# Performance work log

Measured on AMD Instinct MI355X. Metric: run time of the kernel, lower is better.

Reference implementation:

```python
import jax, jax.numpy as jnp
import numpy as np

COMMITMENT_COST = 0.25


def setup_inputs() -> dict:
    key = jax.random.key(0)
    k1, k2 = jax.random.split(key)
    B, T, D = 32, 256, 512
    K = 8192
    x = jax.random.normal(k1, (B, T, D), dtype=jnp.float32)
    # nn.Embedding init: uniform(-1/K, 1/K)
    embeddings = jax.random.uniform(k2, (K, D), dtype=jnp.float32,
                                    minval=-1.0 / K, maxval=1.0 / K)
    return {"x": x, "embeddings": embeddings}


def reference(x, embeddings):
    orig_shape = x.shape
    D = orig_shape[-1]
    x_flat = x.reshape(-1, D)                      # [N, D]

    # squared Euclidean distances via expansion (argmin-equivalent to cdist)
    x_sq = jnp.sum(x_flat * x_flat, axis=1, keepdims=True)     # [N, 1]
    e_sq = jnp.sum(embeddings * embeddings, axis=1)            # [K]
    dots = jnp.einsum('nd,kd->nk', x_flat, embeddings)         # [N, K]
    distances = x_sq - 2.0 * dots + e_sq[None, :]              # [N, K]

    indices = jnp.argmin(distances, axis=1)                    # [N]
    quantized = embeddings[indices].reshape(orig_shape)        # [..., D]
    indices = indices.reshape(orig_shape[:-1])

    commitment_loss = jnp.mean((x - jax.lax.stop_gradient(quantized)) ** 2) * COMMITMENT_COST
    codebook_loss = jnp.mean((quantized - jax.lax.stop_gradient(x)) ** 2)
    total_loss = commitment_loss + codebook_loss

    # straight-through estimator
    quantized_st = x + jax.lax.stop_gradient(quantized - x)
    return quantized_st, indices, commitment_loss, codebook_loss, total_loss
```

## Files before the change

### kernel.cpp

```cpp
#include <hip/hip_runtime.h>

#define N_ROWS 8192
#define K_CODES 8192
#define D_DIM 512

typedef unsigned long long u64;

__global__ __launch_bounds__(256) void vq_sq(const float* __restrict__ x,
                                             const float* __restrict__ emb,
                                             float* __restrict__ x_sq,
                                             float* __restrict__ e_sq) {
  const int t = threadIdx.x;
  const int wave = t >> 6, l = t & 63;
  const int half = l >> 5, ll = l & 31;
  const int q = ll >> 3, j = ll & 7;
  const int row = blockIdx.x * 8 + wave * 2 + half;
  const float* p =
      (row < N_ROWS) ? (x + (size_t)row * D_DIM)
                     : (emb + (size_t)(row - N_ROWS) * D_DIM);
  const float v0 = p[128 * q + j];
  float r = __fmul_rn(v0, v0);
#pragma unroll
  for (int i = 1; i < 16; ++i) {
    const float v = p[128 * q + 8 * i + j];
    r = __fadd_rn(r, __fmul_rn(v, v));
  }
  r = __fadd_rn(r, __shfl_xor(r, 1, 64));
  r = __fadd_rn(r, __shfl_xor(r, 2, 64));
  r = __fadd_rn(r, __shfl_xor(r, 4, 64));
  r = __fadd_rn(r, __shfl_xor(r, 8, 64));
  r = __fadd_rn(r, __shfl_xor(r, 16, 64));
  if (ll == 0) {
    if (row < N_ROWS) x_sq[row] = r;
    else e_sq[row - N_ROWS] = r;
  }
}

__device__ __forceinline__ void compute_chunk16(const float* __restrict__ esb,
                                                const float* __restrict__ xw,
                                                int dd0, int lane,
                                                float (&acc)[8][4]) {
  const int lbase = lane * 16;
  const int lm = (lane >> 1) & 3;
#pragma unroll
  for (int g = 0; g < 4; ++g) {
    const float* p = esb + lbase + 4 * (g ^ lm);
    const float4 ev0 = *reinterpret_cast<const float4*>(p);
    const float4 ev1 = *reinterpret_cast<const float4*>(p + 1024);
    const float4 ev2 = *reinterpret_cast<const float4*>(p + 2048);
    const float4 ev3 = *reinterpret_cast<const float4*>(p + 3072);
#pragma unroll
    for (int r = 0; r < 8; ++r) {
      const float4 xv =
          *reinterpret_cast<const float4*>(xw + r * D_DIM + dd0 + 4 * g);
      float a0 = acc[r][0], a1 = acc[r][1], a2 = acc[r][2], a3 = acc[r][3];
      a0 = __fmaf_rn(xv.x, ev0.x, a0);
      a0 = __fmaf_rn(xv.y, ev0.y, a0);
      a0 = __fmaf_rn(xv.z, ev0.z, a0);
      a0 = __fmaf_rn(xv.w, ev0.w, a0);
      a1 = __fmaf_rn(xv.x, ev1.x, a1);
      a1 = __fmaf_rn(xv.y, ev1.y, a1);
      a1 = __fmaf_rn(xv.z, ev1.z, a1);
      a1 = __fmaf_rn(xv.w, ev1.w, a1);
      a2 = __fmaf_rn(xv.x, ev2.x, a2);
      a2 = __fmaf_rn(xv.y, ev2.y, a2);
      a2 = __fmaf_rn(xv.z, ev2.z, a2);
      a2 = __fmaf_rn(xv.w, ev2.w, a2);
      a3 = __fmaf_rn(xv.x, ev3.x, a3);
      a3 = __fmaf_rn(xv.y, ev3.y, a3);
      a3 = __fmaf_rn(xv.z, ev3.z, a3);
      a3 = __fmaf_rn(xv.w, ev3.w, a3);
      acc[r][0] = a0; acc[r][1] = a1; acc[r][2] = a2; acc[r][3] = a3;
    }
  }
}

#define STAGE(BUF, ESRC)                                                       \
  do {                                                                         \
    __builtin_amdgcn_global_load_lds(                                          \
        (const __attribute__((address_space(1))) void*)(ESRC),                 \
        (__attribute__((address_space(3))) void*)(&es[BUF][4 * t]), 16, 0, 0); \
    __builtin_amdgcn_global_load_lds(                                          \
        (const __attribute__((address_space(1))) void*)((ESRC) + 64 * D_DIM),  \
        (__attribute__((address_space(3))) void*)(&es[BUF][4 * t + 1024]),     \
        16, 0, 0);                                                             \
    __builtin_amdgcn_global_load_lds(                                          \
        (const __attribute__((address_space(1))) void*)((ESRC) + 128 * D_DIM), \
        (__attribute__((address_space(3))) void*)(&es[BUF][4 * t + 2048]),     \
        16, 0, 0);                                                             \
    __builtin_amdgcn_global_load_lds(                                          \
        (const __attribute__((address_space(1))) void*)((ESRC) + 192 * D_DIM), \
        (__attribute__((address_space(3))) void*)(&es[BUF][4 * t + 3072]),     \
        16, 0, 0);                                                             \
  } while (0)

__global__ __launch_bounds__(256, 2) void vq_dist(
    const float* __restrict__ x, const float* __restrict__ e,
    const float* __restrict__ x_sq, const float* __restrict__ e_sq,
    u64* __restrict__ slots) {
  __shared__ float es[2][4096];

  const int t = threadIdx.x;
  const int lane = t & 63;
  const int w = t >> 6;

  const int bx = blockIdx.x;
  const int swz = (bx & 7) * 1024 + (bx >> 3);
  const int kb = swz >> 8;
  const int nb = swz & 255;
  const int k0 = kb * 256;
  const int n0w = __builtin_amdgcn_readfirstlane(nb * 32 + w * 8);
  const float* xw = x + (size_t)n0w * D_DIM;

  const float* esrc =
      e + (size_t)(k0 + (t >> 2)) * D_DIM + 4 * ((t & 3) ^ ((t >> 3) & 3));

  float accA[8][4], accB[8][4];
#pragma unroll
  for (int r = 0; r < 8; ++r)
#pragma unroll
    for (int j = 0; j < 4; ++j) { accA[r][j] = 0.0f; accB[r][j] = 0.0f; }

  STAGE(0, esrc);
  asm volatile("s_waitcnt vmcnt(0)" ::: "memory");
  __syncthreads();

#pragma unroll 1
  for (int c = 0; c < 24; ++c) {
    STAGE((c + 1) & 1, esrc + (c + 1) * 16);
    compute_chunk16(&es[c & 1][0], xw, c * 16, lane, accA);
    asm volatile("s_waitcnt vmcnt(0)" ::: "memory");
    __syncthreads();
  }
#pragma unroll 1
  for (int c = 24; c < 32; ++c) {
    if (c < 31) STAGE((c + 1) & 1, esrc + (c + 1) * 16);
    compute_chunk16(&es[c & 1][0], xw, c * 16, lane, accB);
    asm volatile("s_waitcnt vmcnt(0)" ::: "memory");
    __syncthreads();
  }

  const float4 xsqa = *reinterpret_cast<const float4*>(x_sq + n0w);
  const float4 xsqb = *reinterpret_cast<const float4*>(x_sq + n0w + 4);
  const float xsq[8] = {xsqa.x, xsqa.y, xsqa.z, xsqa.w,
                        xsqb.x, xsqb.y, xsqb.z, xsqb.w};
  const int klane = k0 + lane;
  const float esqv[4] = {e_sq[klane], e_sq[klane + 64], e_sq[klane + 128],
                         e_sq[klane + 192]};

#pragma unroll
  for (int r = 0; r < 8; ++r) {
    u64 best = ~0ULL;
#pragma unroll
    for (int j = 0; j < 4; ++j) {
      float dot = __fadd_rn(accA[r][j], accB[r][j]);
      float dist = __fadd_rn(__fsub_rn(xsq[r], __fmul_rn(2.0f, dot)), esqv[j]);
      unsigned int b = __float_as_uint(dist);
      unsigned int sb = (b & 0x80000000u) ? ~b : (b | 0x80000000u);
      u64 key = ((u64)sb << 32) | (unsigned)(klane + 64 * j);
      best = best < key ? best : key;
    }
#pragma unroll
    for (int off = 32; off > 0; off >>= 1) {
      u64 o = __shfl_xor((unsigned long long)best, off, 64);
      best = best < o ? best : o;
    }
    if (lane == 0) atomicMin(&slots[n0w + r], best);
  }
}

__global__ __launch_bounds__(256) void vq_out(
    const float* __restrict__ x, const float* __restrict__ e,
    const u64* __restrict__ slots, float* __restrict__ out_q,
    float* __restrict__ out_idx, double* __restrict__ loss_part) {
  const int t = threadIdx.x;
  const int w = t >> 6, lane = t & 63;
  const int n = blockIdx.x * 4 + w;
  const int idx = (int)(slots[n] & 0xFFFFFFFFULL);
  const float4* qr = (const float4*)(e + (size_t)idx * D_DIM);
  const float4* xr = (const float4*)(x + (size_t)n * D_DIM);
  float4* outr = (float4*)(out_q + (size_t)n * D_DIM);
  double s = 0.0;
#pragma unroll
  for (int i = 0; i < 2; ++i) {
    const int d4 = lane * 2 + i;
    float4 q = qr[d4];
    float4 xv = xr[d4];
    outr[d4] = q;
    double d0 = (double)xv.x - (double)q.x;
    double d1 = (double)xv.y - (double)q.y;
    double d2 = (double)xv.z - (double)q.z;
    double d3 = (double)xv.w - (double)q.w;
    s += d0 * d0 + d1 * d1 + d2 * d2 + d3 * d3;
  }
  for (int off = 32; off > 0; off >>= 1) s += __shfl_down(s, off, 64);
  if (lane == 0) {
    out_idx[n] = (float)idx;
    atomicAdd(&loss_part[(n * 37) & 255], s);
  }
}

__global__ void vq_loss(const double* __restrict__ loss_part,
                        float* __restrict__ out_s) {
  __shared__ double sm[256];
  const int t = threadIdx.x;
  sm[t] = loss_part[t];
  __syncthreads();
  for (int off = 128; off > 0; off >>= 1) {
    if (t < off) sm[t] += sm[t + off];
    __syncthreads();
  }
  if (t == 0) {
    double m = sm[0] / (double)(N_ROWS * D_DIM);
    out_s[0] = (float)(0.25 * m);
    out_s[1] = (float)m;
    out_s[2] = (float)(1.25 * m);
  }
}

extern "C" void kernel_launch(void* const* d_in, const int* in_sizes, int n_in,
                              void* d_out, int out_size, void* d_ws, size_t ws_size,
                              hipStream_t stream) {
  const float* x = (const float*)d_in[0];
  const float* emb = (const float*)d_in[1];
  float* out = (float*)d_out;

  u64* slots = (u64*)d_ws;
  float* x_sq = (float*)((char*)d_ws + 65536);
  float* e_sq = (float*)((char*)d_ws + 98304);
  double* loss_part = (double*)((char*)d_ws + 131072);

  hipMemsetAsync(d_ws, 0xFF, 65536, stream);
  hipMemsetAsync(loss_part, 0, 256 * sizeof(double), stream);

  vq_sq<<<2048, 256, 0, stream>>>(x, emb, x_sq, e_sq);
  vq_dist<<<8192, 256, 0, stream>>>(x, emb, x_sq, e_sq, slots);
  vq_out<<<N_ROWS / 4, 256, 0, stream>>>(x, emb, slots, out,
                                         out + N_ROWS * D_DIM, loss_part);
  vq_loss<<<1, 256, 0, stream>>>(loss_part, out + N_ROWS * D_DIM + N_ROWS);
}
```

Baseline: 874.5 us.

## Swap operand roles in distance kernel: stage x rows in LDS, broadcast codes

The distance kernel now stages a 256-row tile of x through LDS and has each wave broadcast 8 codebook rows from global memory, rather than staging 256 codes and broadcasting x rows. The block tile changes from 32 rows × 256 codes to 256 rows × 32 codes. The argmin reduction moves from cross-lane shuffles over codes to in-register minima over 8 codes, followed by a shared-memory atomicMin and one global atomicMin per row per block. This changes the global atomic count and the access and reuse pattern of the two operands, at the cost of many more global atomics per row overall (256 code blocks per row instead of 32).

```diff
diff --git a/kernel.cpp b/kernel.cpp
--- a/kernel.cpp
+++ b/kernel.cpp
@@ -36,61 +36,64 @@
   }
 }
 
-__device__ __forceinline__ void compute_chunk16(const float* __restrict__ esb,
-                                                const float* __restrict__ xw,
+__device__ __forceinline__ void compute_chunk16(const float* __restrict__ xsb,
+                                                const float* __restrict__ ew,
                                                 int dd0, int lane,
                                                 float (&acc)[8][4]) {
   const int lbase = lane * 16;
   const int lm = (lane >> 1) & 3;
 #pragma unroll
   for (int g = 0; g < 4; ++g) {
-    const float* p = esb + lbase + 4 * (g ^ lm);
-    const float4 ev0 = *reinterpret_cast<const float4*>(p);
-    const float4 ev1 = *reinterpret_cast<const float4*>(p + 1024);
-    const float4 ev2 = *reinterpret_cast<const float4*>(p + 2048);
-    const float4 ev3 = *reinterpret_cast<const float4*>(p + 3072);
+    const float* p = xsb + lbase + 4 * (g ^ lm);
+    const float4 xv0 = *reinterpret_cast<const float4*>(p);
+    const float4 xv1 = *reinterpret_cast<const float4*>(p + 1024);
+    const float4 xv2 = *reinterpret_cast<const float4*>(p + 2048);
+    const float4 xv3 = *reinterpret_cast<const float4*>(p + 3072);
 #pragma unroll
     for (int r = 0; r < 8; ++r) {
-      const float4 xv =
-          *reinterpret_cast<const float4*>(xw + r * D_DIM + dd0 + 4 * g);
+      const float* eq = ew + r * D_DIM + dd0 + 4 * g;
+      const float e0 = eq[0];
+      const float e1 = eq[1];
+      const float e2 = eq[2];
+      const float e3 = eq[3];
       float a0 = acc[r][0], a1 = acc[r][1], a2 = acc[r][2], a3 = acc[r][3];
-      a0 = __fmaf_rn(xv.x, ev0.x, a0);
-      a0 = __fmaf_rn(xv.y, ev0.y, a0);
-      a0 = __fmaf_rn(xv.z, ev0.z, a0);
-      a0 = __fmaf_rn(xv.w, ev0.w, a0);
-      a1 = __fmaf_rn(xv.x, ev1.x, a1);
-      a1 = __fmaf_rn(xv.y, ev1.y, a1);
-      a1 = __fmaf_rn(xv.z, ev1.z, a1);
-      a1 = __fmaf_rn(xv.w, ev1.w, a1);
-      a2 = __fmaf_rn(xv.x, ev2.x, a2);
-      a2 = __fmaf_rn(xv.y, ev2.y, a2);
-      a2 = __fmaf_rn(xv.z, ev2.z, a2);
-      a2 = __fmaf_rn(xv.w, ev2.w, a2);
-      a3 = __fmaf_rn(xv.x, ev3.x, a3);
-      a3 = __fmaf_rn(xv.y, ev3.y, a3);
-      a3 = __fmaf_rn(xv.z, ev3.z, a3);
-      a3 = __fmaf_rn(xv.w, ev3.w, a3);
+      a0 = __fmaf_rn(xv0.x, e0, a0);
+      a0 = __fmaf_rn(xv0.y, e1, a0);
+      a0 = __fmaf_rn(xv0.z, e2, a0);
+      a0 = __fmaf_rn(xv0.w, e3, a0);
+      a1 = __fmaf_rn(xv1.x, e0, a1);
+      a1 = __fmaf_rn(xv1.y, e1, a1);
+      a1 = __fmaf_rn(xv1.z, e2, a1);
+      a1 = __fmaf_rn(xv1.w, e3, a1);
+      a2 = __fmaf_rn(xv2.x, e0, a2);
+      a2 = __fmaf_rn(xv2.y, e1, a2);
+      a2 = __fmaf_rn(xv2.z, e2, a2);
+      a2 = __fmaf_rn(xv2.w, e3, a2);
+      a3 = __fmaf_rn(xv3.x, e0, a3);
+      a3 = __fmaf_rn(xv3.y, e1, a3);
+      a3 = __fmaf_rn(xv3.z, e2, a3);
+      a3 = __fmaf_rn(xv3.w, e3, a3);
       acc[r][0] = a0; acc[r][1] = a1; acc[r][2] = a2; acc[r][3] = a3;
     }
   }
 }
 
-#define STAGE(BUF, ESRC)                                                       \
+#define STAGE(BUF, XSRC)                                                       \
   do {                                                                         \
     __builtin_amdgcn_global_load_lds(                                          \
-        (const __attribute__((address_space(1))) void*)(ESRC),                 \
-        (__attribute__((address_space(3))) void*)(&es[BUF][4 * t]), 16, 0, 0); \
-    __builtin_amdgcn_global_load_lds(                                          \
-        (const __attribute__((address_space(1))) void*)((ESRC) + 64 * D_DIM),  \
-        (__attribute__((address_space(3))) void*)(&es[BUF][4 * t + 1024]),     \
+        (const __attribute__((address_space(1))) void*)(XSRC),                 \
+        (__attribute__((address_space(3))) void*)(&xs[BUF][4 * t]), 16, 0, 0); \
+    __builtin_amdgcn_global_load_lds(                                          \
+        (const __attribute__((address_space(1))) void*)((XSRC) + 64 * D_DIM),  \
+        (__attribute__((address_space(3))) void*)(&xs[BUF][4 * t + 1024]),     \
         16, 0, 0);                                                             \
     __builtin_amdgcn_global_load_lds(                                          \
-        (const __attribute__((address_space(1))) void*)((ESRC) + 128 * D_DIM), \
-        (__attribute__((address_space(3))) void*)(&es[BUF][4 * t + 2048]),     \
+        (const __attribute__((address_space(1))) void*)((XSRC) + 128 * D_DIM), \
+        (__attribute__((address_space(3))) void*)(&xs[BUF][4 * t + 2048]),     \
         16, 0, 0);                                                             \
     __builtin_amdgcn_global_load_lds(                                          \
-        (const __attribute__((address_space(1))) void*)((ESRC) + 192 * D_DIM), \
-        (__attribute__((address_space(3))) void*)(&es[BUF][4 * t + 3072]),     \
+        (const __attribute__((address_space(1))) void*)((XSRC) + 192 * D_DIM), \
+        (__attribute__((address_space(3))) void*)(&xs[BUF][4 * t + 3072]),     \
         16, 0, 0);                                                             \
   } while (0)
 
@@ -98,22 +101,28 @@
     const float* __restrict__ x, const float* __restrict__ e,
     const float* __restrict__ x_sq, const float* __restrict__ e_sq,
     u64* __restrict__ slots) {
-  __shared__ float es[2][4096];
+  __shared__ float xs[2][4096];
+  __shared__ u64 rowmin[256];
 
   const int t = threadIdx.x;
   const int lane = t & 63;
   const int w = t >> 6;
 
   const int bx = blockIdx.x;
-  const int swz = (bx & 7) * 1024 + (bx >> 3);
-  const int kb = swz >> 8;
-  const int nb = swz & 255;
-  const int k0 = kb * 256;
-  const int n0w = __builtin_amdgcn_readfirstlane(nb * 32 + w * 8);
-  const float* xw = x + (size_t)n0w * D_DIM;
-
-  const float* esrc =
-      e + (size_t)(k0 + (t >> 2)) * D_DIM + 4 * ((t & 3) ^ ((t >> 3) & 3));
+  const int xcd = bx & 7;
+  const int s = bx >> 3;
+  const int kb = xcd * 32 + (s >> 5);
+  const int np = s & 31;
+  const int k0 = kb * 32;
+  const int n0b = np * 256;
+
+  const int kw = __builtin_amdgcn_readfirstlane(k0 + w * 8);
+  const float* ew = e + (size_t)kw * D_DIM;
+
+  const float* xsrc =
+      x + (size_t)(n0b + (t >> 2)) * D_DIM + 4 * ((t & 3) ^ ((t >> 3) & 3));
+
+  rowmin[t] = ~0ULL;
 
   float accA[8][4], accB[8][4];
 #pragma unroll
@@ -121,52 +130,47 @@
 #pragma unroll
     for (int j = 0; j < 4; ++j) { accA[r][j] = 0.0f; accB[r][j] = 0.0f; }
 
-  STAGE(0, esrc);
+  STAGE(0, xsrc);
   asm volatile("s_waitcnt vmcnt(0)" ::: "memory");
   __syncthreads();
 
 #pragma unroll 1
   for (int c = 0; c < 24; ++c) {
-    STAGE((c + 1) & 1, esrc + (c + 1) * 16);
-    compute_chunk16(&es[c & 1][0], xw, c * 16, lane, accA);
+    STAGE((c + 1) & 1, xsrc + (c + 1) * 16);
+    compute_chunk16(&xs[c & 1][0], ew, c * 16, lane, accA);
     asm volatile("s_waitcnt vmcnt(0)" ::: "memory");
     __syncthreads();
   }
 #pragma unroll 1
   for (int c = 24; c < 32; ++c) {
-    if (c < 31) STAGE((c + 1) & 1, esrc + (c + 1) * 16);
-    compute_chunk16(&es[c & 1][0], xw, c * 16, lane, accB);
+    if (c < 31) STAGE((c + 1) & 1, xsrc + (c + 1) * 16);
+    compute_chunk16(&xs[c & 1][0], ew, c * 16, lane, accB);
     asm volatile("s_waitcnt vmcnt(0)" ::: "memory");
     __syncthreads();
   }
 
-  const float4 xsqa = *reinterpret_cast<const float4*>(x_sq + n0w);
-  const float4 xsqb = *reinterpret_cast<const float4*>(x_sq + n0w + 4);
-  const float xsq[8] = {xsqa.x, xsqa.y, xsqa.z, xsqa.w,
-                        xsqb.x, xsqb.y, xsqb.z, xsqb.w};
-  const int klane = k0 + lane;
-  const float esqv[4] = {e_sq[klane], e_sq[klane + 64], e_sq[klane + 128],
-                         e_sq[klane + 192]};
-
-#pragma unroll
-  for (int r = 0; r < 8; ++r) {
+  const float xsqv[4] = {x_sq[n0b + lane], x_sq[n0b + lane + 64],
+                         x_sq[n0b + lane + 128], x_sq[n0b + lane + 192]};
+  float esq[8];
+#pragma unroll
+  for (int r = 0; r < 8; ++r) esq[r] = e_sq[kw + r];
+
+#pragma unroll
+  for (int j = 0; j < 4; ++j) {
     u64 best = ~0ULL;
 #pragma unroll
-    for (int j = 0; j < 4; ++j) {
+    for (int r = 0; r < 8; ++r) {
       float dot = __fadd_rn(accA[r][j], accB[r][j]);
-      float dist = __fadd_rn(__fsub_rn(xsq[r], __fmul_rn(2.0f, dot)), esqv[j]);
+      float dist = __fadd_rn(__fsub_rn(xsqv[j], __fmul_rn(2.0f, dot)), esq[r]);
       unsigned int b = __float_as_uint(dist);
       unsigned int sb = (b & 0x80000000u) ? ~b : (b | 0x80000000u);
-      u64 key = ((u64)sb << 32) | (unsigned)(klane + 64 * j);
+      u64 key = ((u64)sb << 32) | (unsigned)(kw + r);
       best = best < key ? best : key;
     }
-#pragma unroll
-    for (int off = 32; off > 0; off >>= 1) {
-      u64 o = __shfl_xor((unsigned long long)best, off, 64);
-      best = best < o ? best : o;
-    }
-    if (lane == 0) atomicMin(&slots[n0w + r], best);
-  }
+    atomicMin(&rowmin[lane + 64 * j], best);
+  }
+  __syncthreads();
+  atomicMin(&slots[n0b + t], rowmin[t]);
 }
 
 __global__ __launch_bounds__(256) void vq_out(
```

New measurement: 1.004 ms. 1.15x slower.
